# Kernel tuning notes

Hardware: AMD Instinct MI355X
Metric: run time of the kernel (lower is better)

The kernel has to match this reference:

```python
import jax, jax.numpy as jnp
import numpy as np

NEG_SLOPE = 0.2  # LeakyReLU(0.2) on the final Dense


def setup_inputs() -> dict:
    key = jax.random.key(0)
    k1, k2, k3, k4 = jax.random.split(key, 4)
    B, D = 256, 65536          # batch, input voxel dim
    N, G = 41, 2048            # n_groups, group size (overlapping allowed)
    O, E = 256, 512            # per-group output dim, embed_dim
    x = jax.random.normal(k1, (B, D), dtype=jnp.float32)
    group_idx = jax.random.randint(k2, (N, G), 0, D, dtype=jnp.int32)
    # He-normal-ish init for the per-group Dense weights
    W = jax.random.normal(k3, (N, G, O), dtype=jnp.float32) * np.float32(np.sqrt(2.0 / G))
    b = jnp.zeros((N, O), dtype=jnp.float32)
    W3 = jax.random.normal(k4, (N * O, E), dtype=jnp.float32) * np.float32(np.sqrt(2.0 / (N * O)))
    b3 = jnp.zeros((E,), dtype=jnp.float32)
    return {"x": x, "group_idx": group_idx, "W": W, "b": b, "W3": W3, "b3": b3}


def reference(x, group_idx, W, b, W3, b3):
    B = x.shape[0]
    # per-group gather: (B, N, G)
    g = x[:, group_idx]
    # N parallel Dense layers as one grouped GEMM: (B, N, O)
    h = jnp.einsum('bng,ngo->bno', g, W) + b
    # concat along feature axis -> (B, N*O); dropout is identity at inference
    h = h.reshape(B, -1)
    # final Dense + LeakyReLU(0.2)
    out = h @ W3 + b3
    return jnp.where(out >= 0, out, NEG_SLOPE * out)
```

## Files before the change

kernel.cpp:

```cpp
#include <hip/hip_runtime.h>
#include <hip/hip_bf16.h>

#define NB 256
#define DD 65536
#define NN 41
#define GG 2048
#define OO 256
#define NO 10496
#define EE 512
#define NEG_SLOPE 0.2f

typedef __attribute__((ext_vector_type(8))) short bf16x8;
typedef __attribute__((ext_vector_type(4))) float f32x4;
typedef unsigned int u32;

__device__ __forceinline__ void gl_lds16(const __hip_bfloat16* gsrc, __hip_bfloat16* lds) {
    __builtin_amdgcn_global_load_lds((const __attribute__((address_space(1))) u32*)gsrc,
                                     (__attribute__((address_space(3))) u32*)lds, 16, 0, 0);
}

__device__ __forceinline__ u32 pack_bf2(float lo, float hi) {
    u32 a = (u32)__bfloat16_as_ushort(__float2bfloat16(lo));
    u32 b = (u32)__bfloat16_as_ushort(__float2bfloat16(hi));
    return a | (b << 16);
}

__global__ __launch_bounds__(256) void transpose_w3_k(const float* __restrict__ W3,
                                                      __hip_bfloat16* __restrict__ W3t) {
    __shared__ u32 tb[64 * 128];
    int rem = blockIdx.x;
    int kc0 = (rem >> 3) * 256;
    int o0 = (rem & 7) * 64;
    const int K = NO, Oc = EE;
    int t = threadIdx.x;
    int p = t & 127;
    int oh = (t >> 7) * 32;
    const float* r0 = W3 + (size_t)(kc0 + 2 * p) * Oc + o0 + oh;
    const float* r1 = r0 + Oc;
#pragma unroll
    for (int c = 0; c < 8; ++c) {
        float4 a = *(const float4*)&r0[c * 4];
        float4 b = *(const float4*)&r1[c * 4];
        tb[(oh + c * 4 + 0) * 128 + p] = pack_bf2(a.x, b.x);
        tb[(oh + c * 4 + 1) * 128 + p] = pack_bf2(a.y, b.y);
        tb[(oh + c * 4 + 2) * 128 + p] = pack_bf2(a.z, b.z);
        tb[(oh + c * 4 + 3) * 128 + p] = pack_bf2(a.w, b.w);
    }
    __syncthreads();
    int w = t >> 6, l = t & 63;
    int lr = l >> 5;
    int ls = l & 31;
#pragma unroll
    for (int j = 0; j < 8; ++j) {
        int o = j * 8 + w * 2 + lr;
        uint4 v = *(const uint4*)&tb[o * 128 + ls * 4];
        *(uint4*)&W3t[(size_t)(o0 + o) * K + kc0 + ls * 8] = v;
    }
}

__global__ __launch_bounds__(1024) void gather_full_k(const float* __restrict__ x,
                                                      const int* __restrict__ idx,
                                                      __hip_bfloat16* __restrict__ g) {
    extern __shared__ __hip_bfloat16 xr[];
    int b = blockIdx.x;
    int t = threadIdx.x;
    const float4* xv = (const float4*)(x + (size_t)b * DD);
#pragma unroll
    for (int i = 0; i < 16; ++i) {
        float4 v = xv[t + 1024 * i];
        short4 p;
        p.x = (short)__bfloat16_as_ushort(__float2bfloat16(v.x));
        p.y = (short)__bfloat16_as_ushort(__float2bfloat16(v.y));
        p.z = (short)__bfloat16_as_ushort(__float2bfloat16(v.z));
        p.w = (short)__bfloat16_as_ushort(__float2bfloat16(v.w));
        *(short4*)&xr[(t + 1024 * i) * 4] = p;
    }
    __syncthreads();
    const int4* idx4 = (const int4*)idx;
    for (int u = t; u < NN * GG / 4; u += 1024) {
        int4 ii = idx4[u];
        int n = u >> 9;
        int k = (u & 511) * 4;
        ushort4 o;
        o.x = __bfloat16_as_ushort(xr[ii.x]);
        o.y = __bfloat16_as_ushort(xr[ii.y]);
        o.z = __bfloat16_as_ushort(xr[ii.z]);
        o.w = __bfloat16_as_ushort(xr[ii.w]);
        *(ushort4*)&g[((size_t)n * NB + b) * GG + k] = o;
    }
}

__global__ __launch_bounds__(512) void gather_half_k(const float* __restrict__ x,
                                                     const int* __restrict__ idx,
                                                     __hip_bfloat16* __restrict__ g) {
    __shared__ __align__(16) __hip_bfloat16 xr[32768];
    int b = blockIdx.x >> 1;
    int h = blockIdx.x & 1;
    int t = threadIdx.x;
    const float4* xv = (const float4*)(x + (size_t)b * DD + h * 32768);
#pragma unroll
    for (int i = 0; i < 16; ++i) {
        float4 v = xv[t + 512 * i];
        short4 p;
        p.x = (short)__bfloat16_as_ushort(__float2bfloat16(v.x));
        p.y = (short)__bfloat16_as_ushort(__float2bfloat16(v.y));
        p.z = (short)__bfloat16_as_ushort(__float2bfloat16(v.z));
        p.w = (short)__bfloat16_as_ushort(__float2bfloat16(v.w));
        *(short4*)&xr[(t + 512 * i) * 4] = p;
    }
    __syncthreads();
    const int4* idx4 = (const int4*)idx;
    for (int u = t; u < NN * GG / 4; u += 512) {
        int4 ii = idx4[u];
        int n = u >> 9;
        int k = (u & 511) * 4;
        __hip_bfloat16* dst = &g[((size_t)n * NB + b) * GG + k];
        if ((ii.x >> 15) == h) dst[0] = xr[ii.x & 32767];
        if ((ii.y >> 15) == h) dst[1] = xr[ii.y & 32767];
        if ((ii.z >> 15) == h) dst[2] = xr[ii.z & 32767];
        if ((ii.w >> 15) == h) dst[3] = xr[ii.w & 32767];
    }
}

__global__ __launch_bounds__(512) void gemm1_k(const __hip_bfloat16* __restrict__ g,
                                               const float* __restrict__ W,
                                               __hip_bfloat16* __restrict__ part1) {
    int bid0 = blockIdx.x;
    int bid = (bid0 & 7) * 41 + (bid0 >> 3);
    int s = bid & 3;
    int o0 = ((bid >> 2) & 1) * 128;
    int n = bid >> 3;
    const __hip_bfloat16* srcA = g + (size_t)n * NB * GG + s * 512;
    const float* srcB = W + ((size_t)n * GG + s * 512) * OO + o0;
    __shared__ __align__(16) __hip_bfloat16 lA[2][256 * 32];
    __shared__ __align__(16) u32 lB[2][128 * 16];
    int t = threadIdx.x;
    int lane = t & 63, w = t >> 6;
    int mw = (w >> 1) * 64, ow = (w & 1) * 64;
    int lrow = lane & 15, quad = lane >> 4;
    int r0 = t >> 2, q0 = (t & 3) * 8;
    int bp = (t >> 4) & 15;
    int boq8 = t & 15;
    int hi = w >> 2;
    int cb = boq8 * 8 + hi * 4;
    int pw = bp ^ ((boq8 & 3) << 2);
    const float* wb0 = srcB + (size_t)(2 * bp) * OO + cb;
    f32x4 acc[4][4] = {};

    {
        float4 a0 = *(const float4*)&wb0[0];
        float4 b0 = *(const float4*)&wb0[OO];
        u32* d = &lB[0][0];
        d[(cb + 0) * 16 + pw] = pack_bf2(a0.x, b0.x);
        d[(cb + 1) * 16 + pw] = pack_bf2(a0.y, b0.y);
        d[(cb + 2) * 16 + pw] = pack_bf2(a0.z, b0.z);
        d[(cb + 3) * 16 + pw] = pack_bf2(a0.w, b0.w);
    }
    gl_lds16(srcA + (size_t)r0 * GG + q0, &lA[0][t * 8]);
    gl_lds16(srcA + (size_t)(r0 + 128) * GG + q0, &lA[0][(t + 512) * 8]);
    __syncthreads();
#pragma unroll 1
    for (int it = 0; it < 16; ++it) {
        int cur = it & 1;
        float4 a0, b0;
        bool pf = (it + 1 < 16);
        if (pf) {
            int k1 = (it + 1) * 32;
            const float* wn = wb0 + (size_t)k1 * OO;
            a0 = *(const float4*)&wn[0];
            b0 = *(const float4*)&wn[OO];
            gl_lds16(srcA + (size_t)r0 * GG + k1 + q0, &lA[1 - cur][t * 8]);
            gl_lds16(srcA + (size_t)(r0 + 128) * GG + k1 + q0, &lA[1 - cur][(t + 512) * 8]);
        }
        bf16x8 af[4];
#pragma unroll
        for (int fm = 0; fm < 4; ++fm)
            af[fm] = *(const bf16x8*)&lA[cur][(mw + fm * 16 + lrow) * 32 + quad * 8];
        const u32* lbu = &lB[cur][0];
#pragma unroll
        for (int fn = 0; fn < 4; ++fn) {
            int orow = ow + fn * 16 + lrow;
            int fsw = ((orow >> 3) & 3) << 2;
            bf16x8 bfr = *(const bf16x8*)&lbu[orow * 16 + (quad * 4 ^ fsw)];
#pragma unroll
            for (int fm = 0; fm < 4; ++fm)
                acc[fm][fn] = __builtin_amdgcn_mfma_f32_16x16x32_bf16(af[fm], bfr, acc[fm][fn], 0, 0, 0);
        }
        if (pf) {
            u32* d = &lB[1 - cur][0];
            d[(cb + 0) * 16 + pw] = pack_bf2(a0.x, b0.x);
            d[(cb + 1) * 16 + pw] = pack_bf2(a0.y, b0.y);
            d[(cb + 2) * 16 + pw] = pack_bf2(a0.z, b0.z);
            d[(cb + 3) * 16 + pw] = pack_bf2(a0.w, b0.w);
        }
        __syncthreads();
    }
#pragma unroll
    for (int fm = 0; fm < 4; ++fm) {
#pragma unroll
        for (int fn = 0; fn < 4; ++fn) {
            int col = o0 + ow + fn * 16 + lrow;
#pragma unroll
            for (int r = 0; r < 4; ++r) {
                int row = mw + fm * 16 + quad * 4 + r;
                part1[((size_t)s * NB + row) * NO + n * OO + col] = __float2bfloat16(acc[fm][fn][r]);
            }
        }
    }
}

__global__ __launch_bounds__(256) void combine1_k(const __hip_bfloat16* __restrict__ part1,
                                                  const float* __restrict__ bias,
                                                  __hip_bfloat16* __restrict__ h) {
    int j4 = blockIdx.x * 256 + threadIdx.x;
    int jj = j4 % (NO / 4);
    float4 a = ((const float4*)bias)[jj];
#pragma unroll
    for (int s = 0; s < 4; ++s) {
        ushort4 p = *(const ushort4*)&part1[(size_t)s * NB * NO + (size_t)j4 * 4];
        a.x += __bfloat162float(__ushort_as_bfloat16(p.x));
        a.y += __bfloat162float(__ushort_as_bfloat16(p.y));
        a.z += __bfloat162float(__ushort_as_bfloat16(p.z));
        a.w += __bfloat162float(__ushort_as_bfloat16(p.w));
    }
    ushort4 o;
    o.x = __bfloat16_as_ushort(__float2bfloat16(a.x));
    o.y = __bfloat16_as_ushort(__float2bfloat16(a.y));
    o.z = __bfloat16_as_ushort(__float2bfloat16(a.z));
    o.w = __bfloat16_as_ushort(__float2bfloat16(a.w));
    *(ushort4*)&h[(size_t)j4 * 4] = o;
}

__global__ __launch_bounds__(256) void gemm2_k(const __hip_bfloat16* __restrict__ h,
                                               const __hip_bfloat16* __restrict__ W3t,
                                               float* __restrict__ part) {
    int bid0 = blockIdx.x;
    int bid = (bid0 & 7) * 82 + (bid0 >> 3);
    int e0 = (bid & 7) * 64;
    int m0 = ((bid >> 3) & 1) * 128;
    int s = bid >> 4;
    const __hip_bfloat16* srcA = h + (size_t)m0 * NO + s * 256;
    const __hip_bfloat16* srcB = W3t + (size_t)e0 * NO + s * 256;
    __shared__ __align__(16) __hip_bfloat16 lA[2][128 * 32];
    __shared__ __align__(16) __hip_bfloat16 lB[2][64 * 32];
    int t = threadIdx.x;
    int lane = t & 63, w = t >> 6;
    int mw = (w >> 1) * 64, ew = (w & 1) * 32;
    int lrow = lane & 15, quad = lane >> 4;
    int rA = t >> 2, qA = (t & 3) * 8;
    int rB = t >> 2, qB = (t & 3) * 8;
    f32x4 acc[4][2] = {};

    gl_lds16(srcA + (size_t)rA * NO + qA, &lA[0][t * 8]);
    gl_lds16(srcA + (size_t)(rA + 64) * NO + qA, &lA[0][(t + 256) * 8]);
    gl_lds16(srcB + (size_t)(rB & 63) * NO + qB, &lB[0][t * 8]);
    __syncthreads();
#pragma unroll 1
    for (int it = 0; it < 8; ++it) {
        int cur = it & 1;
        if (it + 1 < 8) {
            int k1 = (it + 1) * 32;
            gl_lds16(srcA + (size_t)rA * NO + k1 + qA, &lA[1 - cur][t * 8]);
            gl_lds16(srcA + (size_t)(rA + 64) * NO + k1 + qA, &lA[1 - cur][(t + 256) * 8]);
            gl_lds16(srcB + (size_t)(rB & 63) * NO + k1 + qB, &lB[1 - cur][t * 8]);
        }
        bf16x8 af[4];
#pragma unroll
        for (int fm = 0; fm < 4; ++fm)
            af[fm] = *(const bf16x8*)&lA[cur][(mw + fm * 16 + lrow) * 32 + quad * 8];
#pragma unroll
        for (int fn = 0; fn < 2; ++fn) {
            bf16x8 bfr = *(const bf16x8*)&lB[cur][(ew + fn * 16 + lrow) * 32 + quad * 8];
#pragma unroll
            for (int fm = 0; fm < 4; ++fm)
                acc[fm][fn] = __builtin_amdgcn_mfma_f32_16x16x32_bf16(af[fm], bfr, acc[fm][fn], 0, 0, 0);
        }
        __syncthreads();
    }
#pragma unroll
    for (int fm = 0; fm < 4; ++fm) {
#pragma unroll
        for (int fn = 0; fn < 2; ++fn) {
            int e = e0 + ew + fn * 16 + lrow;
#pragma unroll
            for (int r = 0; r < 4; ++r) {
                int row = m0 + mw + fm * 16 + quad * 4 + r;
                part[((size_t)s * NB + row) * EE + e] = acc[fm][fn][r];
            }
        }
    }
}

__global__ __launch_bounds__(128) void reduce_k(const float* __restrict__ part,
                                                const float* __restrict__ b3,
                                                float* __restrict__ out) {
    int j = blockIdx.x * 128 + threadIdx.x;
    float4 a = make_float4(0.f, 0.f, 0.f, 0.f);
    for (int s = 0; s < NN; ++s) {
        float4 v = ((const float4*)part)[(size_t)s * (NB * EE / 4) + j];
        a.x += v.x; a.y += v.y; a.z += v.z; a.w += v.w;
    }
    float4 bv = ((const float4*)b3)[j & 127];
    a.x += bv.x; a.y += bv.y; a.z += bv.z; a.w += bv.w;
    a.x = a.x >= 0.f ? a.x : NEG_SLOPE * a.x;
    a.y = a.y >= 0.f ? a.y : NEG_SLOPE * a.y;
    a.z = a.z >= 0.f ? a.z : NEG_SLOPE * a.z;
    a.w = a.w >= 0.f ? a.w : NEG_SLOPE * a.w;
    ((float4*)out)[j] = a;
}

extern "C" void kernel_launch(void* const* d_in, const int* in_sizes, int n_in,
                              void* d_out, int out_size, void* d_ws, size_t ws_size,
                              hipStream_t stream) {
    const float* x = (const float*)d_in[0];
    const int* idx = (const int*)d_in[1];
    const float* W = (const float*)d_in[2];
    const float* bias = (const float*)d_in[3];
    const float* W3 = (const float*)d_in[4];
    const float* b3 = (const float*)d_in[5];
    float* out = (float*)d_out;

    char* ws = (char*)d_ws;
    const size_t g_off = 0;
    const size_t g_sz = (size_t)NN * NB * GG * 2;
    const size_t wt_off = g_off + g_sz;
    const size_t wt_sz = (size_t)NN * GG * OO * 2;
    const size_t w3t_off = wt_off + wt_sz;
    const size_t w3t_sz = (size_t)NO * EE * 2;
    const size_t h_off = w3t_off + w3t_sz;
    const size_t h_sz = (size_t)NB * NO * 2;
    const size_t p_off = h_off + h_sz;

    __hip_bfloat16* g = (__hip_bfloat16*)(ws + g_off);
    __hip_bfloat16* W3t = (__hip_bfloat16*)(ws + w3t_off);
    __hip_bfloat16* h = (__hip_bfloat16*)(ws + h_off);
    __hip_bfloat16* part1 = (__hip_bfloat16*)(ws + wt_off);
    float* part = (float*)(ws + p_off);

    transpose_w3_k<<<dim3(NN * 8), 256, 0, stream>>>(W3, W3t);
    hipError_t aerr = hipFuncSetAttribute(reinterpret_cast<const void*>(gather_full_k),
                                          hipFuncAttributeMaxDynamicSharedMemorySize, 131072);
    if (aerr == hipSuccess) {
        gather_full_k<<<dim3(NB), 1024, 131072, stream>>>(x, idx, g);
    } else {
        gather_half_k<<<dim3(512), 512, 0, stream>>>(x, idx, g);
    }
    gemm1_k<<<dim3(328), 512, 0, stream>>>(g, W, part1);
    combine1_k<<<dim3(NB * NO / 4 / 256), 256, 0, stream>>>(part1, bias, h);
    gemm2_k<<<dim3(656), 256, 0, stream>>>(h, W3t, part);
    reduce_k<<<dim3(256), 128, 0, stream>>>(part, b3, out);
}
```

Measured before the change: 261.2 us.

## Fuse W3 transpose into gather kernel and register-prefetch gemm1 two stages ahead

Merges the W3 transpose into the gather kernel as extra blocks, saving one launch and letting the small transpose overlap with the gather. In gemm1, the async global_load_lds path for A is replaced with register loads issued two iterations ahead and stored to LDS after the MMA, in an unrolled double-buffered schedule. The deeper prefetch is meant to hide global latency, at the cost of more registers and a plain LDS store for A instead of the direct-to-LDS load. The transpose blocks now reserve 128KB of dynamic LDS each, which may limit how many blocks run concurrently.

New measurement: 263.4 us. Within noise of the previous version (+0.9%).

```diff
diff --git a/kernel.cpp b/kernel.cpp
--- a/kernel.cpp
+++ b/kernel.cpp
@@ -31,12 +31,11 @@
     int rem = blockIdx.x;
     int kc0 = (rem >> 3) * 256;
     int o0 = (rem & 7) * 64;
-    const int K = NO, Oc = EE;
     int t = threadIdx.x;
     int p = t & 127;
     int oh = (t >> 7) * 32;
-    const float* r0 = W3 + (size_t)(kc0 + 2 * p) * Oc + o0 + oh;
-    const float* r1 = r0 + Oc;
+    const float* r0 = W3 + (size_t)(kc0 + 2 * p) * EE + o0 + oh;
+    const float* r1 = r0 + EE;
 #pragma unroll
     for (int c = 0; c < 8; ++c) {
         float4 a = *(const float4*)&r0[c * 4];
@@ -54,39 +53,69 @@
     for (int j = 0; j < 8; ++j) {
         int o = j * 8 + w * 2 + lr;
         uint4 v = *(const uint4*)&tb[o * 128 + ls * 4];
-        *(uint4*)&W3t[(size_t)(o0 + o) * K + kc0 + ls * 8] = v;
-    }
-}
-
-__global__ __launch_bounds__(1024) void gather_full_k(const float* __restrict__ x,
-                                                      const int* __restrict__ idx,
-                                                      __hip_bfloat16* __restrict__ g) {
+        *(uint4*)&W3t[(size_t)(o0 + o) * NO + kc0 + ls * 8] = v;
+    }
+}
+
+__global__ __launch_bounds__(1024) void prep_k(const float* __restrict__ x,
+                                               const int* __restrict__ idx,
+                                               const float* __restrict__ W3,
+                                               __hip_bfloat16* __restrict__ g,
+                                               __hip_bfloat16* __restrict__ W3t) {
     extern __shared__ __hip_bfloat16 xr[];
-    int b = blockIdx.x;
-    int t = threadIdx.x;
-    const float4* xv = (const float4*)(x + (size_t)b * DD);
-#pragma unroll
-    for (int i = 0; i < 16; ++i) {
-        float4 v = xv[t + 1024 * i];
-        short4 p;
-        p.x = (short)__bfloat16_as_ushort(__float2bfloat16(v.x));
-        p.y = (short)__bfloat16_as_ushort(__float2bfloat16(v.y));
-        p.z = (short)__bfloat16_as_ushort(__float2bfloat16(v.z));
-        p.w = (short)__bfloat16_as_ushort(__float2bfloat16(v.w));
-        *(short4*)&xr[(t + 1024 * i) * 4] = p;
-    }
-    __syncthreads();
-    const int4* idx4 = (const int4*)idx;
-    for (int u = t; u < NN * GG / 4; u += 1024) {
-        int4 ii = idx4[u];
-        int n = u >> 9;
-        int k = (u & 511) * 4;
-        ushort4 o;
-        o.x = __bfloat16_as_ushort(xr[ii.x]);
-        o.y = __bfloat16_as_ushort(xr[ii.y]);
-        o.z = __bfloat16_as_ushort(xr[ii.z]);
-        o.w = __bfloat16_as_ushort(xr[ii.w]);
-        *(ushort4*)&g[((size_t)n * NB + b) * GG + k] = o;
+    int t = threadIdx.x;
+    if (blockIdx.x < NB) {
+        int b = blockIdx.x;
+        const float4* xv = (const float4*)(x + (size_t)b * DD);
+#pragma unroll
+        for (int i = 0; i < 16; ++i) {
+            float4 v = xv[t + 1024 * i];
+            short4 p;
+            p.x = (short)__bfloat16_as_ushort(__float2bfloat16(v.x));
+            p.y = (short)__bfloat16_as_ushort(__float2bfloat16(v.y));
+            p.z = (short)__bfloat16_as_ushort(__float2bfloat16(v.z));
+            p.w = (short)__bfloat16_as_ushort(__float2bfloat16(v.w));
+            *(short4*)&xr[(t + 1024 * i) * 4] = p;
+        }
+        __syncthreads();
+        const int4* idx4 = (const int4*)idx;
+        for (int u = t; u < NN * GG / 4; u += 1024) {
+            int4 ii = idx4[u];
+            int n = u >> 9;
+            int k = (u & 511) * 4;
+            ushort4 o;
+            o.x = __bfloat16_as_ushort(xr[ii.x]);
+            o.y = __bfloat16_as_ushort(xr[ii.y]);
+            o.z = __bfloat16_as_ushort(xr[ii.z]);
+            o.w = __bfloat16_as_ushort(xr[ii.w]);
+            *(ushort4*)&g[((size_t)n * NB + b) * GG + k] = o;
+        }
+    } else {
+        int c = blockIdx.x - NB;
+        int kc0 = (c >> 3) * 256;
+        int o0 = (c & 7) * 64;
+        u32* tb = (u32*)xr;
+        int p = t & 127;
+        int oh = (t >> 7) * 8;
+        const float* r0 = W3 + (size_t)(kc0 + 2 * p) * EE + o0 + oh;
+        const float* r1 = r0 + EE;
+#pragma unroll
+        for (int cc = 0; cc < 2; ++cc) {
+            float4 a = *(const float4*)&r0[cc * 4];
+            float4 b = *(const float4*)&r1[cc * 4];
+            tb[(oh + cc * 4 + 0) * 128 + p] = pack_bf2(a.x, b.x);
+            tb[(oh + cc * 4 + 1) * 128 + p] = pack_bf2(a.y, b.y);
+            tb[(oh + cc * 4 + 2) * 128 + p] = pack_bf2(a.z, b.z);
+            tb[(oh + cc * 4 + 3) * 128 + p] = pack_bf2(a.w, b.w);
+        }
+        __syncthreads();
+        int o = t >> 4;
+        int ls = t & 15;
+        uint4 v0 = *(const uint4*)&tb[o * 128 + ls * 4];
+        uint4 v1 = *(const uint4*)&tb[o * 128 + (ls + 16) * 4];
+        __hip_bfloat16* drow = &W3t[(size_t)(o0 + o) * NO + kc0];
+        *(uint4*)&drow[ls * 8] = v0;
+        *(uint4*)&drow[(ls + 16) * 8] = v1;
     }
 }
 
@@ -144,57 +173,64 @@
     int hi = w >> 2;
     int cb = boq8 * 8 + hi * 4;
     int pw = bp ^ ((boq8 & 3) << 2);
+    const __hip_bfloat16* aR = srcA + (size_t)r0 * GG + q0;
+    const __hip_bfloat16* aS = srcA + (size_t)(r0 + 128) * GG + q0;
     const float* wb0 = srcB + (size_t)(2 * bp) * OO + cb;
     f32x4 acc[4][4] = {};
 
-    {
-        float4 a0 = *(const float4*)&wb0[0];
-        float4 b0 = *(const float4*)&wb0[OO];
-        u32* d = &lB[0][0];
-        d[(cb + 0) * 16 + pw] = pack_bf2(a0.x, b0.x);
-        d[(cb + 1) * 16 + pw] = pack_bf2(a0.y, b0.y);
-        d[(cb + 2) * 16 + pw] = pack_bf2(a0.z, b0.z);
-        d[(cb + 3) * 16 + pw] = pack_bf2(a0.w, b0.w);
-    }
-    gl_lds16(srcA + (size_t)r0 * GG + q0, &lA[0][t * 8]);
-    gl_lds16(srcA + (size_t)(r0 + 128) * GG + q0, &lA[0][(t + 512) * 8]);
+    uint4 axl, axh; float4 bxa, bxb;
+    uint4 ayl, ayh; float4 bya, byb;
+
+#define LOADX(kk) { axl = *(const uint4*)&aR[kk]; axh = *(const uint4*)&aS[kk]; \
+                    const float* wn_ = wb0 + (size_t)(kk) * OO; \
+                    bxa = *(const float4*)&wn_[0]; bxb = *(const float4*)&wn_[OO]; }
+#define LOADY(kk) { ayl = *(const uint4*)&aR[kk]; ayh = *(const uint4*)&aS[kk]; \
+                    const float* wn_ = wb0 + (size_t)(kk) * OO; \
+                    bya = *(const float4*)&wn_[0]; byb = *(const float4*)&wn_[OO]; }
+#define STOREX(buf) { *(uint4*)&lA[buf][t * 8] = axl; *(uint4*)&lA[buf][(t + 512) * 8] = axh; \
+                      u32* d_ = &lB[buf][0]; \
+                      d_[(cb + 0) * 16 + pw] = pack_bf2(bxa.x, bxb.x); \
+                      d_[(cb + 1) * 16 + pw] = pack_bf2(bxa.y, bxb.y); \
+                      d_[(cb + 2) * 16 + pw] = pack_bf2(bxa.z, bxb.z); \
+                      d_[(cb + 3) * 16 + pw] = pack_bf2(bxa.w, bxb.w); }
+#define STOREY(buf) { *(uint4*)&lA[buf][t * 8] = ayl; *(uint4*)&lA[buf][(t + 512) * 8] = ayh; \
+                      u32* d_ = &lB[buf][0]; \
+                      d_[(cb + 0) * 16 + pw] = pack_bf2(bya.x, byb.x); \
+                      d_[(cb + 1) * 16 + pw] = pack_bf2(bya.y, byb.y); \
+                      d_[(cb + 2) * 16 + pw] = pack_bf2(bya.z, byb.z); \
+                      d_[(cb + 3) * 16 + pw] = pack_bf2(bya.w, byb.w); }
+#define MMA(buf) { bf16x8 af[4]; \
+    _Pragma("unroll") for (int fm = 0; fm < 4; ++fm) \
+        af[fm] = *(const bf16x8*)&lA[buf][(mw + fm * 16 + lrow) * 32 + quad * 8]; \
+    const u32* lbu = &lB[buf][0]; \
+    _Pragma("unroll") for (int fn = 0; fn < 4; ++fn) { \
+        int orow = ow + fn * 16 + lrow; \
+        int fsw = ((orow >> 3) & 3) << 2; \
+        bf16x8 bfr = *(const bf16x8*)&lbu[orow * 16 + (quad * 4 ^ fsw)]; \
+        _Pragma("unroll") for (int fm = 0; fm < 4; ++fm) \
+            acc[fm][fn] = __builtin_amdgcn_mfma_f32_16x16x32_bf16(af[fm], bfr, acc[fm][fn], 0, 0, 0); } }
+
+    LOADX(0);
+    LOADY(32);
+    STOREX(0);
     __syncthreads();
 #pragma unroll 1
-    for (int it = 0; it < 16; ++it) {
-        int cur = it & 1;
-        float4 a0, b0;
-        bool pf = (it + 1 < 16);
-        if (pf) {
-            int k1 = (it + 1) * 32;
-            const float* wn = wb0 + (size_t)k1 * OO;
-            a0 = *(const float4*)&wn[0];
-            b0 = *(const float4*)&wn[OO];
-            gl_lds16(srcA + (size_t)r0 * GG + k1 + q0, &lA[1 - cur][t * 8]);
-            gl_lds16(srcA + (size_t)(r0 + 128) * GG + k1 + q0, &lA[1 - cur][(t + 512) * 8]);
-        }
-        bf16x8 af[4];
-#pragma unroll
-        for (int fm = 0; fm < 4; ++fm)
-            af[fm] = *(const bf16x8*)&lA[cur][(mw + fm * 16 + lrow) * 32 + quad * 8];
-        const u32* lbu = &lB[cur][0];
-#pragma unroll
-        for (int fn = 0; fn < 4; ++fn) {
-            int orow = ow + fn * 16 + lrow;
-            int fsw = ((orow >> 3) & 3) << 2;
-            bf16x8 bfr = *(const bf16x8*)&lbu[orow * 16 + (quad * 4 ^ fsw)];
-#pragma unroll
-            for (int fm = 0; fm < 4; ++fm)
-                acc[fm][fn] = __builtin_amdgcn_mfma_f32_16x16x32_bf16(af[fm], bfr, acc[fm][fn], 0, 0, 0);
-        }
-        if (pf) {
-            u32* d = &lB[1 - cur][0];
-            d[(cb + 0) * 16 + pw] = pack_bf2(a0.x, b0.x);
-            d[(cb + 1) * 16 + pw] = pack_bf2(a0.y, b0.y);
-            d[(cb + 2) * 16 + pw] = pack_bf2(a0.z, b0.z);
-            d[(cb + 3) * 16 + pw] = pack_bf2(a0.w, b0.w);
-        }
-        __syncthreads();
-    }
+    for (int j = 0; j < 8; ++j) {
+        int itE = 2 * j;
+        if (itE + 2 < 16) LOADX((itE + 2) * 32);
+        MMA(0);
+        STOREY(1);
+        __syncthreads();
+        if (itE + 3 < 16) LOADY((itE + 3) * 32);
+        MMA(1);
+        if (itE + 2 < 16) STOREX(0);
+        __syncthreads();
+    }
+#undef LOADX
+#undef LOADY
+#undef STOREX
+#undef STOREY
+#undef MMA
 #pragma unroll
     for (int fm = 0; fm < 4; ++fm) {
 #pragma unroll
@@ -337,12 +373,12 @@
     __hip_bfloat16* part1 = (__hip_bfloat16*)(ws + wt_off);
     float* part = (float*)(ws + p_off);
 
-    transpose_w3_k<<<dim3(NN * 8), 256, 0, stream>>>(W3, W3t);
-    hipError_t aerr = hipFuncSetAttribute(reinterpret_cast<const void*>(gather_full_k),
+    hipError_t aerr = hipFuncSetAttribute(reinterpret_cast<const void*>(prep_k),
                                           hipFuncAttributeMaxDynamicSharedMemorySize, 131072);
     if (aerr == hipSuccess) {
-        gather_full_k<<<dim3(NB), 1024, 131072, stream>>>(x, idx, g);
+        prep_k<<<dim3(NB + NN * 8), 1024, 131072, stream>>>(x, idx, W3, g, W3t);
     } else {
+        transpose_w3_k<<<dim3(NN * 8), 256, 0, stream>>>(W3, W3t);
         gather_half_k<<<dim3(512), 512, 0, stream>>>(x, idx, g);
     }
     gemm1_k<<<dim3(328), 512, 0, stream>>>(g, W, part1);
```
